# Optimization experiments

Measured on AMD Instinct MI355X. Metric: run time of the kernel, lower is better.

Reference implementation:

```python
import jax, jax.numpy as jnp
import numpy as np

B_, L, S_IN, S_OUT, Z_IN, Z_OUT = 2, 768, 1280, 32, 1, 32
D_INNER, D_STATE, D_CONV, DT_RANK = 64, 16, 4, 2  # expand=2 -> d_inner=64; dt_rank=ceil(32/16)=2


def setup_inputs() -> dict:
    key = jax.random.key(0)
    ks = jax.random.split(key, 12)
    p = lambda i, shape, scale=0.02: jax.random.normal(ks[i], shape, jnp.float32) * scale
    return dict(
        s=jax.random.normal(ks[0], (B_, L, S_IN), jnp.float32),
        z=jax.random.normal(ks[1], (B_, L, L, Z_IN), jnp.float32),
        s_proj_w=p(2, (S_OUT, S_IN)), s_proj_b=jnp.zeros((S_OUT,), jnp.float32),
        z_proj_w=p(3, (Z_OUT, Z_IN)), z_proj_b=jnp.zeros((Z_OUT,), jnp.float32),
        in_proj_w=p(4, (2 * D_INNER, S_OUT)),
        conv_w=p(5, (D_INNER, D_CONV)), conv_b=jnp.zeros((D_INNER,), jnp.float32),
        x_proj_w=p(6, (DT_RANK + 2 * D_STATE, D_INNER)),
        dt_proj_w=p(7, (D_INNER, DT_RANK)), dt_proj_b=p(8, (D_INNER,), 1.0),
        A_log=jnp.log(jnp.broadcast_to(jnp.arange(1, D_STATE + 1, dtype=jnp.float32), (D_INNER, D_STATE))),
        D=jnp.ones((D_INNER,), jnp.float32),
        out_proj_w=p(9, (S_OUT, D_INNER)),
    )


def mamba(u, in_proj_w, conv_w, conv_b, x_proj_w, dt_proj_w, dt_proj_b, A_log, D, out_proj_w):
    # u: [b, l, d_model]
    b, l, _ = u.shape
    xz = u @ in_proj_w.T                      # [b, l, 2*d_inner]
    x, gate = jnp.split(xz, 2, axis=-1)
    # causal depthwise conv1d, kernel D_CONV, then SiLU
    xp = jnp.pad(x, ((0, 0), (D_CONV - 1, 0), (0, 0)))
    x = sum(xp[:, k:k + l, :] * conv_w[:, k] for k in range(D_CONV)) + conv_b
    x = jax.nn.silu(x)
    x_dbl = x @ x_proj_w.T                    # [b, l, dt_rank + 2*d_state]
    dt, Bm, Cm = jnp.split(x_dbl, [DT_RANK, DT_RANK + D_STATE], axis=-1)
    dt = jax.nn.softplus(dt @ dt_proj_w.T + dt_proj_b)   # [b, l, d_inner]
    A = -jnp.exp(A_log)                       # [d_inner, d_state]
    dA = jnp.exp(dt[..., None] * A)           # [b, l, d, n]
    dBu = dt[..., None] * Bm[:, :, None, :] * x[..., None]  # [b, l, d, n]

    def step(h, ins):
        dA_t, dBu_t, C_t = ins
        h = dA_t * h + dBu_t                  # [b, d, n]
        return h, jnp.einsum('bdn,bn->bd', h, C_t)

    h0 = jnp.zeros((b, D_INNER, D_STATE), u.dtype)
    _, ys = jax.lax.scan(step, h0, (jnp.swapaxes(dA, 0, 1), jnp.swapaxes(dBu, 0, 1), jnp.swapaxes(Cm, 0, 1)))
    y = jnp.swapaxes(ys, 0, 1) + x * D        # D skip connection
    y = y * jax.nn.silu(gate)                 # gated output
    return y @ out_proj_w.T                   # [b, l, d_model]


def reference(s, z, s_proj_w, s_proj_b, z_proj_w, z_proj_b, in_proj_w, conv_w, conv_b,
              x_proj_w, dt_proj_w, dt_proj_b, A_log, D, out_proj_w):
    s_prime = s @ s_proj_w.T + s_proj_b                       # [b, l, 32]
    s_prime = mamba(s_prime, in_proj_w, conv_w, conv_b, x_proj_w,
                    dt_proj_w, dt_proj_b, A_log, D, out_proj_w)
    z_prime = z @ z_proj_w.T + z_proj_b                       # [b, l, l, 32]
    z_prime = z_prime + jnp.einsum('bsf,btf->bstf', s_prime, s_prime)
    return (s_prime, z_prime)
```

## Files before the change

### kernel.cpp

```cpp
#include <hip/hip_runtime.h>
#include <math.h>

#define B_     2
#define L_     768
#define SIN_   1280
#define SOUT_  32
#define DI_    64
#define DST_   16
#define DCONV_ 4
#define DTR_   2
#define NCH    96
#define CH     8


__global__ __launch_bounds__(256) void k_sproj(
    const float* __restrict__ s, const float* __restrict__ spw,
    const float* __restrict__ spb, const float* __restrict__ ipw,
    float* __restrict__ xz)
{
    __shared__ float srow[2][SIN_];
    __shared__ float w2[128 * 33];
    __shared__ float u[2][SOUT_];
    const int tid = threadIdx.x;
    const int row0 = blockIdx.x * 2;

    for (int r = 0; r < 2; ++r) {
        const float4* src = (const float4*)(s + (long)(row0 + r) * SIN_);
        for (int i = tid; i < SIN_ / 4; i += 256)
            ((float4*)srow[r])[i] = src[i];
    }
    for (int i = tid; i < 128 * 32; i += 256)
        w2[(i >> 5) * 33 + (i & 31)] = ipw[i];
    __syncthreads();

    const int f = tid >> 3;
    const int c = tid & 7;
    float p0 = 0.f, p1 = 0.f;
    const float4* w4p = (const float4*)(spw + (long)f * SIN_);
    const float4* a0p = (const float4*)srow[0];
    const float4* a1p = (const float4*)srow[1];
    for (int k4 = c; k4 < SIN_ / 4; k4 += 8) {
        float4 w  = w4p[k4];
        float4 a0 = a0p[k4];
        float4 a1 = a1p[k4];
        p0 = fmaf(a0.x, w.x, fmaf(a0.y, w.y, fmaf(a0.z, w.z, fmaf(a0.w, w.w, p0))));
        p1 = fmaf(a1.x, w.x, fmaf(a1.y, w.y, fmaf(a1.z, w.z, fmaf(a1.w, w.w, p1))));
    }
    #pragma unroll
    for (int m = 1; m <= 4; m <<= 1) {
        p0 += __shfl_xor(p0, m);
        p1 += __shfl_xor(p1, m);
    }
    if (c == 0) {
        float bb = spb[f];
        u[0][f] = p0 + bb;
        u[1][f] = p1 + bb;
    }
    __syncthreads();

    const int j = tid & 127;
    const int r = tid >> 7;
    float acc = 0.f;
    const float* wj = &w2[j * 33];
    #pragma unroll
    for (int k = 0; k < SOUT_; ++k) acc += u[r][k] * wj[k];
    xz[(long)(row0 + r) * 128 + j] = acc;
}

__global__ __launch_bounds__(256) void k_pre(
    const float* __restrict__ xz, const float* __restrict__ convw,
    const float* __restrict__ convb, const float* __restrict__ xpw,
    const float* __restrict__ dtw, const float* __restrict__ dtb,
    const float* __restrict__ Alog,
    float* __restrict__ xs_out, float* __restrict__ dtf_out,
    float* __restrict__ Bws, float* __restrict__ Cws,
    float* __restrict__ Pst, float* __restrict__ Lst)
{
    const int bc = blockIdx.x;
    const int b  = bc / NCH, c = bc - b * NCH;
    const int l0 = c * CH;
    const long rbase = (long)b * L_ + l0;
    const int tid = threadIdx.x;

    __shared__ float sxpw[64][34];
    __shared__ float sdtw[128];
    __shared__ float sxs[CH][DI_];
    __shared__ float sxd[CH][34];
    __shared__ float sdt[CH][DI_];
    __shared__ float sdx[CH][DI_];

    for (int i = tid; i < 34 * 64; i += 256)
        sxpw[i & 63][i >> 6] = xpw[i];
    if (tid < 128) sdtw[tid] = dtw[tid];

    for (int it = tid; it < CH * DI_; it += 256) {
        int r = it >> 6, d = it & 63;
        int l = l0 + r;
        float xc = convb[d];
        #pragma unroll
        for (int k = 0; k < DCONV_; ++k) {
            int ls = l + k - (DCONV_ - 1);
            if (ls >= 0) xc = fmaf(xz[(long)(b * L_ + ls) * 128 + d], convw[d * 4 + k], xc);
        }
        float xv = xc / (1.f + expf(-xc));
        sxs[r][d] = xv;
        xs_out[(rbase + r) * DI_ + d] = xv;
    }
    __syncthreads();

    for (int it = tid; it < CH * 34; it += 256) {
        int r = it / 34, o = it - r * 34;
        float acc = 0.f;
        #pragma unroll
        for (int k = 0; k < DI_; ++k) acc = fmaf(sxs[r][k], sxpw[k][o], acc);
        sxd[r][o] = acc;
    }
    __syncthreads();

    for (int it = tid; it < CH * DI_; it += 256) {
        int r = it >> 6, d = it & 63;
        float dtv = fmaf(sxd[r][0], sdtw[2 * d], fmaf(sxd[r][1], sdtw[2 * d + 1], dtb[d]));
        dtv = dtv > 20.f ? dtv : log1pf(expf(dtv));
        sdt[r][d] = dtv;
        sdx[r][d] = dtv * sxs[r][d];
        dtf_out[(rbase + r) * DI_ + d] = dtv;
    }
    if (tid < CH * DST_) {
        int r = tid >> 4, n = tid & 15;
        Bws[(rbase + r) * DST_ + n] = sxd[r][DTR_ + n];
        Cws[(rbase + r) * DST_ + n] = sxd[r][DTR_ + DST_ + n];
    }
    __syncthreads();

    const int n = tid & 15, g = tid >> 4;
    float P[4], hl[4], A2[4];
    #pragma unroll
    for (int q = 0; q < 4; ++q) {
        int d = g + 16 * q;
        A2[q] = -expf(Alog[d * DST_ + n]) * 1.44269504088896f;
        P[q] = 1.f; hl[q] = 0.f;
    }
    #pragma unroll
    for (int l = 0; l < CH; ++l) {
        float bv = sxd[l][DTR_ + n];
        #pragma unroll
        for (int q = 0; q < 4; ++q) {
            int d = g + 16 * q;
            float a = exp2f(sdt[l][d] * A2[q]);
            P[q] *= a;
            hl[q] = fmaf(a, hl[q], sdx[l][d] * bv);
        }
    }
    const long o0 = (long)bc * 1024 + g * 16 + n;
    #pragma unroll
    for (int q = 0; q < 4; ++q) {
        Pst[o0 + 256 * q] = P[q];
        Lst[o0 + 256 * q] = hl[q];
    }
}

__global__ __launch_bounds__(1024) void k_back(
    const float* __restrict__ dtf, const float* __restrict__ xs,
    const float* __restrict__ Bws, const float* __restrict__ Cws,
    const float* __restrict__ Alog, const float* __restrict__ Pst,
    const float* __restrict__ Lst, const float* __restrict__ xz,
    const float* __restrict__ Dv, const float* __restrict__ opw,
    float* __restrict__ sp)
{
    const int bc = blockIdx.x;
    const int b  = bc / NCH, c = bc - b * NCH;
    const int l0 = c * CH;
    const long rbase = (long)b * L_ + l0;
    const int tid = threadIdx.x;

    __shared__ float sB[CH][DST_], sC[CH][DST_];
    __shared__ float sdt[CH][DI_], sxsS[CH][DI_];
    __shared__ float sy[CH][65];
    __shared__ float sw[64][33];

    if (tid < CH * DI_) {
        sdt[tid >> 6][tid & 63] = dtf[rbase * DI_ + tid];
    } else {
        int t = tid - CH * DI_;
        sxsS[t >> 6][t & 63] = xs[rbase * DI_ + t];
    }
    if (tid < CH * DST_) {
        sB[tid >> 4][tid & 15] = Bws[rbase * DST_ + tid];
    } else if (tid < 2 * CH * DST_) {
        int t = tid - CH * DST_;
        sC[t >> 4][t & 15] = Cws[rbase * DST_ + t];
    }
    for (int i = tid; i < SOUT_ * DI_; i += 1024)
        sw[i & 63][i >> 6] = opw[i];

    float h = 0.f;
    {
        const long ebase = (long)b * NCH * 1024 + tid;
        #pragma unroll 4
        for (int c2 = 0; c2 < c; ++c2) {
            long o = ebase + (long)c2 * 1024;
            h = fmaf(Pst[o], h, Lst[o]);
        }
    }
    const int d = tid >> 4, n = tid & 15;
    float A2 = -expf(Alog[d * DST_ + n]) * 1.44269504088896f;
    __syncthreads();

    #pragma unroll
    for (int l = 0; l < CH; ++l) {
        float dtv = sdt[l][d];
        float a = exp2f(dtv * A2);
        h = fmaf(a, h, dtv * sxsS[l][d] * sB[l][n]);
        float y = h * sC[l][n];
        y += __shfl_xor(y, 1);
        y += __shfl_xor(y, 2);
        y += __shfl_xor(y, 4);
        y += __shfl_xor(y, 8);
        if (n == 0) sy[l][d] = y;
    }
    __syncthreads();

    if (tid < CH * DI_) {
        int r = tid >> 6, dd = tid & 63;
        float g  = xz[(rbase + r) * 128 + DI_ + dd];
        float yv = fmaf(sxsS[r][dd], Dv[dd], sy[r][dd]);
        sy[r][dd] = yv * (g / (1.f + expf(-g)));
    }
    __syncthreads();

    if (tid < CH * SOUT_) {
        int r = tid >> 5, o = tid & 31;
        float acc = 0.f;
        #pragma unroll
        for (int k = 0; k < DI_; ++k) acc = fmaf(sy[r][k], sw[k][o], acc);
        sp[(rbase + r) * SOUT_ + o] = acc;
    }
}

__global__ __launch_bounds__(256) void k_z(
    const float* __restrict__ z, const float* __restrict__ zw,
    const float* __restrict__ zb, const float* __restrict__ sp,
    float* __restrict__ zout)
{
    const int idx = blockIdx.x * 256 + threadIdx.x;
    const int bs  = idx / 6144;
    const int rem = idx - bs * 6144;
    const int t   = rem >> 3;
    const int f4  = rem & 7;
    const int b   = bs / L_;

    float zval = z[(long)bs * L_ + t];
    float4 w4 = ((const float4*)zw)[f4];
    float4 b4 = ((const float4*)zb)[f4];
    float4 ss = ((const float4*)sp)[bs * 8 + f4];
    float4 st = ((const float4*)sp)[(b * L_ + t) * 8 + f4];
    float4 o;
    o.x = zval * w4.x + b4.x + ss.x * st.x;
    o.y = zval * w4.y + b4.y + ss.y * st.y;
    o.z = zval * w4.z + b4.z + ss.z * st.z;
    o.w = zval * w4.w + b4.w + ss.w * st.w;
    ((float4*)zout)[(long)idx] = o;
}

extern "C" void kernel_launch(void* const* d_in, const int* in_sizes, int n_in,
                              void* d_out, int out_size, void* d_ws, size_t ws_size,
                              hipStream_t stream) {
    const float* s     = (const float*)d_in[0];
    const float* z     = (const float*)d_in[1];
    const float* spw   = (const float*)d_in[2];
    const float* spb   = (const float*)d_in[3];
    const float* zw    = (const float*)d_in[4];
    const float* zb    = (const float*)d_in[5];
    const float* ipw   = (const float*)d_in[6];
    const float* convw = (const float*)d_in[7];
    const float* convb = (const float*)d_in[8];
    const float* xpw   = (const float*)d_in[9];
    const float* dtw   = (const float*)d_in[10];
    const float* dtb   = (const float*)d_in[11];
    const float* Alog  = (const float*)d_in[12];
    const float* Dv    = (const float*)d_in[13];
    const float* opw   = (const float*)d_in[14];

    float* out = (float*)d_out;
    float* ws  = (float*)d_ws;
    float* xz  = ws;
    float* xs  = ws + 196608;
    float* dtf = ws + 294912;
    float* Bws = ws + 393216;
    float* Cws = ws + 417792;
    float* Pst = ws + 442368;
    float* Lst = ws + 638976;

    float* sp   = out;
    float* zout = out + 49152;

    k_sproj<<<(B_ * L_) / 2, 256, 0, stream>>>(s, spw, spb, ipw, xz);
    k_pre  <<<B_ * NCH, 256, 0, stream>>>(xz, convw, convb, xpw, dtw, dtb, Alog,
                                          xs, dtf, Bws, Cws, Pst, Lst);
    k_back <<<B_ * NCH, 1024, 0, stream>>>(dtf, xs, Bws, Cws, Alog, Pst, Lst,
                                           xz, Dv, opw, sp);
    k_z    <<<(B_ * L_ * L_ * 8) / 256, 256, 0, stream>>>(z, zw, zb, sp, zout);
}
```

Measured before the change: 258.3 us.

## Fuse s projection and in_proj into the chunk preprocessing kernel

Merges the s_proj/in_proj kernel into the per-chunk pre-scan kernel. Each chunk block recomputes the 32-wide projection for its 8 rows plus a 3-row conv halo, computes the x half and gate half of in_proj in shared memory, and writes only the gate to the workspace. This removes one launch and the global round trip for the xz buffer. In exchange, the grid drops to 192 blocks, each doing a long 1280-wide reduction with 44 accumulators per thread, and the halo rows are computed redundantly, so parallelism and register pressure both get worse.

```diff
diff --git a/kernel.cpp b/kernel.cpp
--- a/kernel.cpp
+++ b/kernel.cpp
@@ -13,107 +13,120 @@
 #define CH     8
 
 
-__global__ __launch_bounds__(256) void k_sproj(
+__global__ __launch_bounds__(256) void k_front(
     const float* __restrict__ s, const float* __restrict__ spw,
     const float* __restrict__ spb, const float* __restrict__ ipw,
-    float* __restrict__ xz)
+    const float* __restrict__ convw, const float* __restrict__ convb,
+    const float* __restrict__ xpw, const float* __restrict__ dtw,
+    const float* __restrict__ dtb, const float* __restrict__ Alog,
+    float* __restrict__ gate_o, float* __restrict__ xs_o,
+    float* __restrict__ dtf_o, float* __restrict__ Bws,
+    float* __restrict__ Cws, float* __restrict__ Pst, float* __restrict__ Lst)
 {
-    __shared__ float srow[2][SIN_];
-    __shared__ float w2[128 * 33];
-    __shared__ float u[2][SOUT_];
-    const int tid = threadIdx.x;
-    const int row0 = blockIdx.x * 2;
-
-    for (int r = 0; r < 2; ++r) {
-        const float4* src = (const float4*)(s + (long)(row0 + r) * SIN_);
-        for (int i = tid; i < SIN_ / 4; i += 256)
-            ((float4*)srow[r])[i] = src[i];
-    }
-    for (int i = tid; i < 128 * 32; i += 256)
-        w2[(i >> 5) * 33 + (i & 31)] = ipw[i];
-    __syncthreads();
-
-    const int f = tid >> 3;
-    const int c = tid & 7;
-    float p0 = 0.f, p1 = 0.f;
-    const float4* w4p = (const float4*)(spw + (long)f * SIN_);
-    const float4* a0p = (const float4*)srow[0];
-    const float4* a1p = (const float4*)srow[1];
-    for (int k4 = c; k4 < SIN_ / 4; k4 += 8) {
-        float4 w  = w4p[k4];
-        float4 a0 = a0p[k4];
-        float4 a1 = a1p[k4];
-        p0 = fmaf(a0.x, w.x, fmaf(a0.y, w.y, fmaf(a0.z, w.z, fmaf(a0.w, w.w, p0))));
-        p1 = fmaf(a1.x, w.x, fmaf(a1.y, w.y, fmaf(a1.z, w.z, fmaf(a1.w, w.w, p1))));
-    }
-    #pragma unroll
-    for (int m = 1; m <= 4; m <<= 1) {
-        p0 += __shfl_xor(p0, m);
-        p1 += __shfl_xor(p1, m);
-    }
-    if (c == 0) {
-        float bb = spb[f];
-        u[0][f] = p0 + bb;
-        u[1][f] = p1 + bb;
-    }
-    __syncthreads();
-
-    const int j = tid & 127;
-    const int r = tid >> 7;
-    float acc = 0.f;
-    const float* wj = &w2[j * 33];
-    #pragma unroll
-    for (int k = 0; k < SOUT_; ++k) acc += u[r][k] * wj[k];
-    xz[(long)(row0 + r) * 128 + j] = acc;
-}
-
-__global__ __launch_bounds__(256) void k_pre(
-    const float* __restrict__ xz, const float* __restrict__ convw,
-    const float* __restrict__ convb, const float* __restrict__ xpw,
-    const float* __restrict__ dtw, const float* __restrict__ dtb,
-    const float* __restrict__ Alog,
-    float* __restrict__ xs_out, float* __restrict__ dtf_out,
-    float* __restrict__ Bws, float* __restrict__ Cws,
-    float* __restrict__ Pst, float* __restrict__ Lst)
-{
-    const int bc = blockIdx.x;
-    const int b  = bc / NCH, c = bc - b * NCH;
-    const int l0 = c * CH;
+    const int bc  = blockIdx.x;
+    const int b   = bc / NCH, c = bc - b * NCH;
+    const int l0  = c * CH;
     const long rbase = (long)b * L_ + l0;
     const int tid = threadIdx.x;
 
+    __shared__ float w2[128 * 33];
     __shared__ float sxpw[64][34];
     __shared__ float sdtw[128];
+    __shared__ float su[11][SOUT_];
+    __shared__ float sx[11][DI_];
     __shared__ float sxs[CH][DI_];
     __shared__ float sxd[CH][34];
     __shared__ float sdt[CH][DI_];
     __shared__ float sdx[CH][DI_];
 
+    for (int i = tid; i < 128 * 32; i += 256)
+        w2[(i >> 5) * 33 + (i & 31)] = ipw[i];
     for (int i = tid; i < 34 * 64; i += 256)
         sxpw[i & 63][i >> 6] = xpw[i];
     if (tid < 128) sdtw[tid] = dtw[tid];
 
+    const int fg = tid >> 5;
+    const int cc = tid & 31;
+    float acc[11][4];
+    #pragma unroll
+    for (int r = 0; r < 11; ++r)
+        #pragma unroll
+        for (int j = 0; j < 4; ++j) acc[r][j] = 0.f;
+
+    {
+        const float4* s4   = (const float4*)s;
+        const float4* spw4 = (const float4*)spw;
+        const long sb4 = ((long)b * L_ + l0 - 3) * (SIN_ / 4);
+        for (int i = 0; i < 10; ++i) {
+            const int k4 = cc + 32 * i;
+            float4 w0 = spw4[(long)(fg     ) * 320 + k4];
+            float4 w1 = spw4[(long)(fg +  8) * 320 + k4];
+            float4 wv = spw4[(long)(fg + 16) * 320 + k4];
+            float4 w3 = spw4[(long)(fg + 24) * 320 + k4];
+            #pragma unroll
+            for (int r = 0; r < 11; ++r) {
+                if (l0 - 3 + r >= 0) {
+                    float4 a = s4[sb4 + (long)r * 320 + k4];
+                    acc[r][0] = fmaf(a.x, w0.x, fmaf(a.y, w0.y, fmaf(a.z, w0.z, fmaf(a.w, w0.w, acc[r][0]))));
+                    acc[r][1] = fmaf(a.x, w1.x, fmaf(a.y, w1.y, fmaf(a.z, w1.z, fmaf(a.w, w1.w, acc[r][1]))));
+                    acc[r][2] = fmaf(a.x, wv.x, fmaf(a.y, wv.y, fmaf(a.z, wv.z, fmaf(a.w, wv.w, acc[r][2]))));
+                    acc[r][3] = fmaf(a.x, w3.x, fmaf(a.y, w3.y, fmaf(a.z, w3.z, fmaf(a.w, w3.w, acc[r][3]))));
+                }
+            }
+        }
+    }
+    #pragma unroll
+    for (int r = 0; r < 11; ++r) {
+        #pragma unroll
+        for (int j = 0; j < 4; ++j) {
+            float v = acc[r][j];
+            v += __shfl_xor(v, 1);  v += __shfl_xor(v, 2);
+            v += __shfl_xor(v, 4);  v += __shfl_xor(v, 8);
+            v += __shfl_xor(v, 16);
+            if (cc == 0) {
+                int f = fg + 8 * j;
+                su[r][f] = (l0 - 3 + r >= 0) ? v + spb[f] : 0.f;
+            }
+        }
+    }
+    __syncthreads();
+
+    for (int it = tid; it < 11 * DI_; it += 256) {
+        int r = it >> 6, j = it & 63;
+        const float* w = &w2[j * 33];
+        float a = 0.f;
+        #pragma unroll
+        for (int k = 0; k < SOUT_; ++k) a = fmaf(su[r][k], w[k], a);
+        sx[r][j] = a;
+    }
+    for (int it = tid; it < CH * DI_; it += 256) {
+        int r = it >> 6, j = it & 63;
+        const float* w = &w2[(64 + j) * 33];
+        float a = 0.f;
+        #pragma unroll
+        for (int k = 0; k < SOUT_; ++k) a = fmaf(su[r + 3][k], w[k], a);
+        gate_o[rbase * DI_ + it] = a;
+    }
+    __syncthreads();
+
     for (int it = tid; it < CH * DI_; it += 256) {
         int r = it >> 6, d = it & 63;
-        int l = l0 + r;
         float xc = convb[d];
         #pragma unroll
-        for (int k = 0; k < DCONV_; ++k) {
-            int ls = l + k - (DCONV_ - 1);
-            if (ls >= 0) xc = fmaf(xz[(long)(b * L_ + ls) * 128 + d], convw[d * 4 + k], xc);
-        }
+        for (int k = 0; k < DCONV_; ++k)
+            xc = fmaf(sx[r + k][d], convw[d * 4 + k], xc);
         float xv = xc / (1.f + expf(-xc));
         sxs[r][d] = xv;
-        xs_out[(rbase + r) * DI_ + d] = xv;
+        xs_o[rbase * DI_ + it] = xv;
     }
     __syncthreads();
 
     for (int it = tid; it < CH * 34; it += 256) {
         int r = it / 34, o = it - r * 34;
-        float acc = 0.f;
-        #pragma unroll
-        for (int k = 0; k < DI_; ++k) acc = fmaf(sxs[r][k], sxpw[k][o], acc);
-        sxd[r][o] = acc;
+        float a = 0.f;
+        #pragma unroll
+        for (int k = 0; k < DI_; ++k) a = fmaf(sxs[r][k], sxpw[k][o], a);
+        sxd[r][o] = a;
     }
     __syncthreads();
 
@@ -123,12 +136,12 @@
         dtv = dtv > 20.f ? dtv : log1pf(expf(dtv));
         sdt[r][d] = dtv;
         sdx[r][d] = dtv * sxs[r][d];
-        dtf_out[(rbase + r) * DI_ + d] = dtv;
+        dtf_o[rbase * DI_ + it] = dtv;
     }
     if (tid < CH * DST_) {
         int r = tid >> 4, n = tid & 15;
-        Bws[(rbase + r) * DST_ + n] = sxd[r][DTR_ + n];
-        Cws[(rbase + r) * DST_ + n] = sxd[r][DTR_ + DST_ + n];
+        Bws[rbase * DST_ + tid] = sxd[r][DTR_ + n];
+        Cws[rbase * DST_ + tid] = sxd[r][DTR_ + DST_ + n];
     }
     __syncthreads();
 
@@ -163,7 +176,7 @@
     const float* __restrict__ dtf, const float* __restrict__ xs,
     const float* __restrict__ Bws, const float* __restrict__ Cws,
     const float* __restrict__ Alog, const float* __restrict__ Pst,
-    const float* __restrict__ Lst, const float* __restrict__ xz,
+    const float* __restrict__ Lst, const float* __restrict__ gate,
     const float* __restrict__ Dv, const float* __restrict__ opw,
     float* __restrict__ sp)
 {
@@ -222,7 +235,7 @@
 
     if (tid < CH * DI_) {
         int r = tid >> 6, dd = tid & 63;
-        float g  = xz[(rbase + r) * 128 + DI_ + dd];
+        float g  = gate[rbase * DI_ + tid];
         float yv = fmaf(sxsS[r][dd], Dv[dd], sy[r][dd]);
         sy[r][dd] = yv * (g / (1.f + expf(-g)));
     }
@@ -233,7 +246,7 @@
         float acc = 0.f;
         #pragma unroll
         for (int k = 0; k < DI_; ++k) acc = fmaf(sy[r][k], sw[k][o], acc);
-        sp[(rbase + r) * SOUT_ + o] = acc;
+        sp[rbase * SOUT_ + tid] = acc;
     }
 }
 
@@ -281,23 +294,23 @@
     const float* Dv    = (const float*)d_in[13];
     const float* opw   = (const float*)d_in[14];
 
-    float* out = (float*)d_out;
-    float* ws  = (float*)d_ws;
-    float* xz  = ws;
-    float* xs  = ws + 196608;
-    float* dtf = ws + 294912;
-    float* Bws = ws + 393216;
-    float* Cws = ws + 417792;
-    float* Pst = ws + 442368;
-    float* Lst = ws + 638976;
+    float* out  = (float*)d_out;
+    float* ws   = (float*)d_ws;
+    float* gate = ws;
+    float* xs   = ws + 98304;
+    float* dtf  = ws + 196608;
+    float* Bws  = ws + 294912;
+    float* Cws  = ws + 319488;
+    float* Pst  = ws + 344064;
+    float* Lst  = ws + 442368;
 
     float* sp   = out;
     float* zout = out + 49152;
 
-    k_sproj<<<(B_ * L_) / 2, 256, 0, stream>>>(s, spw, spb, ipw, xz);
-    k_pre  <<<B_ * NCH, 256, 0, stream>>>(xz, convw, convb, xpw, dtw, dtb, Alog,
-                                          xs, dtf, Bws, Cws, Pst, Lst);
+    k_front<<<B_ * NCH, 256, 0, stream>>>(s, spw, spb, ipw, convw, convb, xpw,
+                                          dtw, dtb, Alog, gate, xs, dtf,
+                                          Bws, Cws, Pst, Lst);
     k_back <<<B_ * NCH, 1024, 0, stream>>>(dtf, xs, Bws, Cws, Alog, Pst, Lst,
-                                           xz, Dv, opw, sp);
+                                           gate, Dv, opw, sp);
     k_z    <<<(B_ * L_ * L_ * 8) / 256, 256, 0, stream>>>(z, zw, zb, sp, zout);
 }
```

Result: slower. 292.1 us (+13.1%).
